# Kernel tuning notes

Measured on AMD Instinct MI355X. Metric: run time of the kernel, lower is better.

Reference implementation:

```python
import jax, jax.numpy as jnp
import numpy as np

B, S, D, H = 2, 2048, 1024, 16
DH = D // H  # head dim = 64


def setup_inputs() -> dict:
    key0 = jax.random.key(0)
    ks = jax.random.split(key0, 12)
    wscale = 0.02
    inp = {
        "query": jax.random.normal(ks[0], (B, S, D), jnp.float32),
        "key": jax.random.normal(ks[1], (B, S, D), jnp.float32),
        "value": jax.random.normal(ks[2], (B, S, D), jnp.float32),
        "mask": jnp.zeros((B, 1, 1, S), jnp.float32),  # 1.0 = masked position
        "Wq": jax.random.normal(ks[3], (D, D), jnp.float32) * wscale,
        "bq": jnp.zeros((D,), jnp.float32),
        "Wk": jax.random.normal(ks[4], (D, D), jnp.float32) * wscale,
        "bk": jnp.zeros((D,), jnp.float32),
        "Wv": jax.random.normal(ks[5], (D, D), jnp.float32) * wscale,
        "bv": jnp.zeros((D,), jnp.float32),
        "Wo": jax.random.normal(ks[6], (D, D), jnp.float32) * wscale,
        "bo": jnp.zeros((D,), jnp.float32),
        "batch_size": B,
    }
    return inp


def _split_heads(x, batch_size):
    # [B, S, D] -> [B, H, S, DH]
    return x.reshape(batch_size, -1, H, DH).transpose(0, 2, 1, 3)


def reference(query, key, value, mask, Wq, bq, Wk, bk, Wv, bv, Wo, bo, batch_size):
    q = _split_heads(query @ Wq + bq, batch_size)  # [B,H,S,DH]
    k = _split_heads(key @ Wk + bk, batch_size)
    v = _split_heads(value @ Wv + bv, batch_size)

    scale = 1.0 / jnp.sqrt(jnp.asarray(DH, q.dtype))
    scores = jnp.einsum("bhqd,bhkd->bhqk", q, k) * scale  # [B,H,S,S]
    scores = scores + mask * jnp.asarray(-1e9, scores.dtype)
    attn = jax.nn.softmax(scores, axis=-1)
    ctx = jnp.einsum("bhqk,bhkd->bhqd", attn, v)  # [B,H,S,DH]

    ctx = ctx.transpose(0, 2, 1, 3).reshape(batch_size, -1, D)  # [B,S,D]
    return ctx @ Wo + bo
```

## Files before the change

kernel.cpp:

```cpp
#include <hip/hip_runtime.h>
#include <hip/hip_bf16.h>

#define BB 2
#define SS 2048
#define DD 1024
#define HH 16
#define DHH 64
#define MM (BB * SS)

typedef unsigned short u16;
using v8s   = __attribute__((ext_vector_type(8))) short;
using f32x4 = __attribute__((ext_vector_type(4))) float;

__device__ __forceinline__ u16 f2bf(float f) {
  unsigned int u = __float_as_uint(f);
  u += 0x7fffu + ((u >> 16) & 1u);
  return (u16)(u >> 16);
}

__device__ __forceinline__ void async_cp16(const u16* g, u16* l) {
  __builtin_amdgcn_global_load_lds(
      (const __attribute__((address_space(1))) unsigned int*)g,
      (__attribute__((address_space(3))) unsigned int*)l, 16, 0, 0);
}

__global__ __launch_bounds__(256) void conv_all(const float* __restrict__ x0,
                                                const float* __restrict__ x1,
                                                const float* __restrict__ x2,
                                                u16* __restrict__ y0,
                                                u16* __restrict__ y1,
                                                u16* __restrict__ y2) {
  const int z = blockIdx.y;
  const float* x = z == 0 ? x0 : (z == 1 ? x1 : x2);
  u16* y = z == 0 ? y0 : (z == 1 ? y1 : y2);
  int i = (blockIdx.x * 256 + threadIdx.x) * 4;
  float4 v = *(const float4*)(x + i);
  ushort4 u;
  u.x = f2bf(v.x); u.y = f2bf(v.y); u.z = f2bf(v.z); u.w = f2bf(v.w);
  *(ushort4*)(y + i) = u;
}

__global__ __launch_bounds__(256) void trans_all(
    const float* __restrict__ W0, const float* __restrict__ W1,
    const float* __restrict__ W2, const float* __restrict__ W3,
    u16* __restrict__ T0, u16* __restrict__ T1,
    u16* __restrict__ T2, u16* __restrict__ T3) {
  const int z = blockIdx.z;
  const float* W = z == 0 ? W0 : (z == 1 ? W1 : (z == 2 ? W2 : W3));
  u16* Wt = z == 0 ? T0 : (z == 1 ? T1 : (z == 2 ? T2 : T3));
  __shared__ u16 T[64][72];
  const int tid = threadIdx.x;
  const int k0 = blockIdx.y * 64, n0 = blockIdx.x * 64;
#pragma unroll
  for (int i = 0; i < 4; i++) {
    int idx = tid + i * 256;
    int r = idx >> 4, c = (idx & 15) * 4;
    float4 x = *(const float4*)(W + (long)(k0 + r) * DD + n0 + c);
    T[c + 0][r] = f2bf(x.x);
    T[c + 1][r] = f2bf(x.y);
    T[c + 2][r] = f2bf(x.z);
    T[c + 3][r] = f2bf(x.w);
  }
  __syncthreads();
#pragma unroll
  for (int i = 0; i < 2; i++) {
    int idx = tid + i * 256;
    int n = idx >> 3, kc = (idx & 7) * 8;
    *(v8s*)(Wt + (long)(n0 + n) * DD + k0 + kc) = *(const v8s*)&T[n][kc];
  }
}

__global__ __launch_bounds__(256, 2) void proj_fused(
    const u16* __restrict__ qb, const u16* __restrict__ kb, const u16* __restrict__ vb,
    const u16* __restrict__ Wqt, const u16* __restrict__ Wkt, const u16* __restrict__ Wvt,
    const float* __restrict__ bq, const float* __restrict__ bk, const float* __restrict__ bv,
    u16* __restrict__ qo, u16* __restrict__ ko, u16* __restrict__ vo) {
  __shared__ u16 As[128 * 32];
  __shared__ u16 Bs[128 * 32];
  const int z = blockIdx.z;
  const u16* A  = z == 0 ? qb : (z == 1 ? kb : vb);
  const u16* Bt = z == 0 ? Wqt : (z == 1 ? Wkt : Wvt);
  const float* bias = z == 0 ? bq : (z == 1 ? bk : bv);
  u16* out = z == 0 ? qo : (z == 1 ? ko : vo);
  const float scale = z == 0 ? 0.125f : 1.0f;

  const int tid = threadIdx.x;
  const int w = tid >> 6, lane = tid & 63;
  const int quad = lane >> 4, lq = lane & 15;
  const int wm = w >> 1, wn = w & 1;
  const int row0 = blockIdx.y * 128, col0 = blockIdx.x * 128;

  f32x4 acc[4][4];
#pragma unroll
  for (int i = 0; i < 4; i++)
#pragma unroll
    for (int j = 0; j < 4; j++)
#pragma unroll
      for (int r = 0; r < 4; r++) acc[i][j][r] = 0.f;

  const int cr = tid >> 2, cc = (tid & 3) * 8;

  for (int k0 = 0; k0 < DD; k0 += 32) {
    __syncthreads();
    async_cp16(A  + (long)(row0 + cr) * DD + k0 + cc,      As + (w * 64) * 8);
    async_cp16(A  + (long)(row0 + 64 + cr) * DD + k0 + cc, As + (256 + w * 64) * 8);
    async_cp16(Bt + (long)(col0 + cr) * DD + k0 + cc,      Bs + (w * 64) * 8);
    async_cp16(Bt + (long)(col0 + 64 + cr) * DD + k0 + cc, Bs + (256 + w * 64) * 8);
    __syncthreads();

    v8s a[4], b[4];
#pragma unroll
    for (int i = 0; i < 4; i++)
      a[i] = *(const v8s*)&As[(wm * 64 + i * 16 + lq) * 32 + quad * 8];
#pragma unroll
    for (int j = 0; j < 4; j++)
      b[j] = *(const v8s*)&Bs[(wn * 64 + j * 16 + lq) * 32 + quad * 8];
#pragma unroll
    for (int i = 0; i < 4; i++)
#pragma unroll
      for (int j = 0; j < 4; j++)
        acc[i][j] = __builtin_amdgcn_mfma_f32_16x16x32_bf16(a[i], b[j], acc[i][j], 0, 0, 0);
  }

#pragma unroll
  for (int i = 0; i < 4; i++)
#pragma unroll
    for (int j = 0; j < 4; j++) {
      int n = col0 + wn * 64 + j * 16 + lq;
      float bi = bias[n];
#pragma unroll
      for (int r = 0; r < 4; r++) {
        int m = row0 + wm * 64 + i * 16 + quad * 4 + r;
        float val = (acc[i][j][r] + bi) * scale;
        int bb = m >> 11, s = m & (SS - 1);
        int hh = n >> 6, d = n & (DHH - 1);
        long off = (z != 2) ? ((long)(bb * HH + hh) * SS + s) * DHH + d
                            : ((long)(bb * HH + hh) * DHH + d) * SS + s;
        out[off] = f2bf(val);
      }
    }
}

__global__ __launch_bounds__(256, 2) void out_gemm(const u16* __restrict__ A,
                                                   const u16* __restrict__ Bt,
                                                   const float* __restrict__ bias,
                                                   float* __restrict__ outp) {
  __shared__ u16 As[64 * 32];
  __shared__ u16 Bs[128 * 32];
  const int tid = threadIdx.x;
  const int w = tid >> 6, lane = tid & 63;
  const int quad = lane >> 4, lq = lane & 15;
  const int wm = w >> 1, wn = w & 1;
  const int row0 = blockIdx.y * 64, col0 = blockIdx.x * 128;

  f32x4 acc[2][4];
#pragma unroll
  for (int i = 0; i < 2; i++)
#pragma unroll
    for (int j = 0; j < 4; j++)
#pragma unroll
      for (int r = 0; r < 4; r++) acc[i][j][r] = 0.f;

  const int cr = tid >> 2, cc = (tid & 3) * 8;

  for (int k0 = 0; k0 < DD; k0 += 32) {
    __syncthreads();
    async_cp16(A  + (long)(row0 + cr) * DD + k0 + cc,      As + (w * 64) * 8);
    async_cp16(Bt + (long)(col0 + cr) * DD + k0 + cc,      Bs + (w * 64) * 8);
    async_cp16(Bt + (long)(col0 + 64 + cr) * DD + k0 + cc, Bs + (256 + w * 64) * 8);
    __syncthreads();

    v8s a[2], b[4];
#pragma unroll
    for (int i = 0; i < 2; i++)
      a[i] = *(const v8s*)&As[(wm * 32 + i * 16 + lq) * 32 + quad * 8];
#pragma unroll
    for (int j = 0; j < 4; j++)
      b[j] = *(const v8s*)&Bs[(wn * 64 + j * 16 + lq) * 32 + quad * 8];
#pragma unroll
    for (int i = 0; i < 2; i++)
#pragma unroll
      for (int j = 0; j < 4; j++)
        acc[i][j] = __builtin_amdgcn_mfma_f32_16x16x32_bf16(a[i], b[j], acc[i][j], 0, 0, 0);
  }

#pragma unroll
  for (int i = 0; i < 2; i++)
#pragma unroll
    for (int j = 0; j < 4; j++) {
      int n = col0 + wn * 64 + j * 16 + lq;
      float bi = bias[n];
#pragma unroll
      for (int r = 0; r < 4; r++) {
        int m = row0 + wm * 32 + i * 16 + quad * 4 + r;
        outp[(long)m * DD + n] = acc[i][j][r] + bi;
      }
    }
}

__global__ __launch_bounds__(256, 2) void attn_flash(
    const u16* __restrict__ qg, const u16* __restrict__ kg,
    const u16* __restrict__ vg, const float* __restrict__ mask,
    u16* __restrict__ ctx) {
  __shared__ u16 Ks[128 * 72];
  __shared__ u16 Vs[64 * 136];
  __shared__ u16 Pts[128 * 136];
  __shared__ float mneg[128];

  const int tid = threadIdx.x;
  const int w = tid >> 6, lane = tid & 63;
  const int quad = lane >> 4, lq = lane & 15;
  const int q0 = blockIdx.x * 128;
  const int h = blockIdx.y, b = blockIdx.z;
  const long hoff = (long)(b * HH + h) * SS * DHH;

  v8s aq[2][2];
#pragma unroll
  for (int qs_ = 0; qs_ < 2; qs_++)
#pragma unroll
    for (int ks_ = 0; ks_ < 2; ks_++)
      aq[qs_][ks_] = *(const v8s*)(qg + hoff +
          (long)(q0 + w * 32 + qs_ * 16 + lq) * DHH + ks_ * 32 + quad * 8);

  f32x4 o[2][4];
  float l_i[2] = {0.f, 0.f};
#pragma unroll
  for (int a = 0; a < 2; a++)
#pragma unroll
    for (int n_ = 0; n_ < 4; n_++)
#pragma unroll
      for (int r = 0; r < 4; r++) o[a][n_][r] = 0.f;

  for (int kv0 = 0; kv0 < SS; kv0 += 128) {
    __syncthreads();
#pragma unroll
    for (int t = 0; t < 4; t++) {
      int c = tid + t * 256;
      *(v8s*)&Ks[(c >> 3) * 72 + (c & 7) * 8] =
          *(const v8s*)(kg + hoff + (long)(kv0 + (c >> 3)) * DHH + (c & 7) * 8);
      *(v8s*)&Vs[(c >> 4) * 136 + (c & 15) * 8] =
          *(const v8s*)(vg + hoff + (long)(c >> 4) * SS + kv0 + (c & 15) * 8);
    }
    if (tid < 32) {
      float4 mm = *(const float4*)(mask + (long)b * SS + kv0 + tid * 4);
      mneg[tid * 4 + 0] = mm.x * -1e9f - 4.0f;
      mneg[tid * 4 + 1] = mm.y * -1e9f - 4.0f;
      mneg[tid * 4 + 2] = mm.z * -1e9f - 4.0f;
      mneg[tid * 4 + 3] = mm.w * -1e9f - 4.0f;
    }
    __syncthreads();

    f32x4 sc[2][8];
#pragma unroll
    for (int qs_ = 0; qs_ < 2; qs_++)
#pragma unroll
      for (int kv_ = 0; kv_ < 8; kv_++)
#pragma unroll
        for (int r = 0; r < 4; r++) sc[qs_][kv_][r] = 0.f;
#pragma unroll
    for (int ks_ = 0; ks_ < 2; ks_++)
#pragma unroll
      for (int kv_ = 0; kv_ < 8; kv_++) {
        v8s ak = *(const v8s*)&Ks[(kv_ * 16 + lq) * 72 + ks_ * 32 + quad * 8];
        sc[0][kv_] = __builtin_amdgcn_mfma_f32_16x16x32_bf16(ak, aq[0][ks_], sc[0][kv_], 0, 0, 0);
        sc[1][kv_] = __builtin_amdgcn_mfma_f32_16x16x32_bf16(ak, aq[1][ks_], sc[1][kv_], 0, 0, 0);
      }

#pragma unroll
    for (int qs_ = 0; qs_ < 2; qs_++) {
      float lsum = 0.f;
      const int prow = (w * 32 + qs_ * 16 + lq) * 136;
#pragma unroll
      for (int kv_ = 0; kv_ < 8; kv_++) {
        f32x4 mv = *(const f32x4*)&mneg[kv_ * 16 + quad * 4];
        float p0 = __expf(sc[qs_][kv_][0] + mv[0]);
        float p1 = __expf(sc[qs_][kv_][1] + mv[1]);
        float p2 = __expf(sc[qs_][kv_][2] + mv[2]);
        float p3 = __expf(sc[qs_][kv_][3] + mv[3]);
        lsum += (p0 + p1) + (p2 + p3);
        ushort4 pk;
        pk.x = f2bf(p0); pk.y = f2bf(p1); pk.z = f2bf(p2); pk.w = f2bf(p3);
        *(ushort4*)&Pts[prow + kv_ * 16 + quad * 4] = pk;
      }
      l_i[qs_] += lsum;
    }

#pragma unroll
    for (int ks2 = 0; ks2 < 4; ks2++) {
      v8s bv[4];
#pragma unroll
      for (int n_ = 0; n_ < 4; n_++)
        bv[n_] = *(const v8s*)&Vs[(n_ * 16 + lq) * 136 + ks2 * 32 + quad * 8];
#pragma unroll
      for (int qs_ = 0; qs_ < 2; qs_++) {
        v8s ap = *(const v8s*)&Pts[(w * 32 + qs_ * 16 + lq) * 136 + ks2 * 32 + quad * 8];
#pragma unroll
        for (int n_ = 0; n_ < 4; n_++)
          o[qs_][n_] = __builtin_amdgcn_mfma_f32_16x16x32_bf16(ap, bv[n_], o[qs_][n_], 0, 0, 0);
      }
    }
  }

#pragma unroll
  for (int qs_ = 0; qs_ < 2; qs_++) {
    float l = l_i[qs_];
    l += __shfl_xor(l, 16);
    l += __shfl_xor(l, 32);
    float inv = 1.0f / l;
    float ir[4];
    ir[0] = __shfl(inv, quad * 4 + 0);
    ir[1] = __shfl(inv, quad * 4 + 1);
    ir[2] = __shfl(inv, quad * 4 + 2);
    ir[3] = __shfl(inv, quad * 4 + 3);
#pragma unroll
    for (int r = 0; r < 4; r++) {
      int s = q0 + w * 32 + qs_ * 16 + quad * 4 + r;
      long base = (long)(b * SS + s) * DD + h * DHH;
#pragma unroll
      for (int n_ = 0; n_ < 4; n_++)
        ctx[base + n_ * 16 + lq] = f2bf(o[qs_][n_][r] * ir[r]);
    }
  }
}

extern "C" void kernel_launch(void* const* d_in, const int* in_sizes, int n_in,
                              void* d_out, int out_size, void* d_ws, size_t ws_size,
                              hipStream_t stream) {
  const float* query = (const float*)d_in[0];
  const float* key   = (const float*)d_in[1];
  const float* value = (const float*)d_in[2];
  const float* mask  = (const float*)d_in[3];
  const float* Wq = (const float*)d_in[4];
  const float* bq = (const float*)d_in[5];
  const float* Wk = (const float*)d_in[6];
  const float* bk = (const float*)d_in[7];
  const float* Wv = (const float*)d_in[8];
  const float* bv = (const float*)d_in[9];
  const float* Wo = (const float*)d_in[10];
  const float* bo = (const float*)d_in[11];

  u16* ws = (u16*)d_ws;
  const long A4 = (long)MM * DD;
  const long W1 = (long)DD * DD;
  u16* qb  = ws;
  u16* kb  = ws + A4;
  u16* vb  = ws + 2 * A4;
  u16* Wqt = ws + 3 * A4;
  u16* Wkt = Wqt + W1;
  u16* Wvt = Wkt + W1;
  u16* Wot = Wvt + W1;
  u16* q_ws   = ws + 3 * A4 + 4 * W1;
  u16* k_ws   = q_ws + A4;
  u16* v_ws   = k_ws + A4;
  u16* ctx_ws = v_ws + A4;

  conv_all<<<dim3(A4 / 1024, 3), 256, 0, stream>>>(query, key, value, qb, kb, vb);
  trans_all<<<dim3(16, 16, 4), 256, 0, stream>>>(Wq, Wk, Wv, Wo, Wqt, Wkt, Wvt, Wot);

  proj_fused<<<dim3(DD / 128, MM / 128, 3), 256, 0, stream>>>(
      qb, kb, vb, Wqt, Wkt, Wvt, bq, bk, bv, q_ws, k_ws, v_ws);

  attn_flash<<<dim3(SS / 128, HH, BB), 256, 0, stream>>>(q_ws, k_ws, v_ws, mask, ctx_ws);

  out_gemm<<<dim3(DD / 128, MM / 64), 256, 0, stream>>>(ctx_ws, Wot, bo, (float*)d_out);
}
```

Measured before the change: 248.7 us.

## Stage projection epilogue through LDS for coalesced stores; use exp2 and packed bf16

The QKV projection epilogue now writes results into a shared-memory tile (aliased with the GEMM staging buffers through a union) and then issues 16-byte coalesced stores in the head-split layout. The V output is written transposed through the tile, which replaces the scattered 2-byte global writes. The attention softmax folds log2(e) into the Q scale and the mask offset so it can use exp2f, and bf16 conversions use the packed hardware conversion intrinsic. The larger shared buffer may reduce occupancy, and the packed conversion's rounding may differ slightly from the manual round-to-nearest-even.

After: 251.8 us. Within noise of the previous version (+1.3%).

```diff
diff --git a/kernel.cpp b/kernel.cpp
--- a/kernel.cpp
+++ b/kernel.cpp
@@ -12,10 +12,17 @@
 using v8s   = __attribute__((ext_vector_type(8))) short;
 using f32x4 = __attribute__((ext_vector_type(4))) float;
 
+#define LOG2E 1.44269504088896340736f
+
 __device__ __forceinline__ u16 f2bf(float f) {
   unsigned int u = __float_as_uint(f);
   u += 0x7fffu + ((u >> 16) & 1u);
   return (u16)(u >> 16);
+}
+
+__device__ __forceinline__ unsigned int pk2(float a, float b) {
+  __hip_bfloat162 h = __float22bfloat162_rn(float2{a, b});
+  return *(unsigned int*)&h;
 }
 
 __device__ __forceinline__ void async_cp16(const u16* g, u16* l) {
@@ -35,9 +42,10 @@
   u16* y = z == 0 ? y0 : (z == 1 ? y1 : y2);
   int i = (blockIdx.x * 256 + threadIdx.x) * 4;
   float4 v = *(const float4*)(x + i);
-  ushort4 u;
-  u.x = f2bf(v.x); u.y = f2bf(v.y); u.z = f2bf(v.z); u.w = f2bf(v.w);
-  *(ushort4*)(y + i) = u;
+  uint2 u;
+  u.x = pk2(v.x, v.y);
+  u.y = pk2(v.z, v.w);
+  *(uint2*)(y + i) = u;
 }
 
 __global__ __launch_bounds__(256) void trans_all(
@@ -75,14 +83,16 @@
     const u16* __restrict__ Wqt, const u16* __restrict__ Wkt, const u16* __restrict__ Wvt,
     const float* __restrict__ bq, const float* __restrict__ bk, const float* __restrict__ bv,
     u16* __restrict__ qo, u16* __restrict__ ko, u16* __restrict__ vo) {
-  __shared__ u16 As[128 * 32];
-  __shared__ u16 Bs[128 * 32];
+  __shared__ union ShU {
+    struct { u16 As[128 * 32]; u16 Bs[128 * 32]; } st;
+    u16 T[128 * 136];
+  } sh;
   const int z = blockIdx.z;
   const u16* A  = z == 0 ? qb : (z == 1 ? kb : vb);
   const u16* Bt = z == 0 ? Wqt : (z == 1 ? Wkt : Wvt);
   const float* bias = z == 0 ? bq : (z == 1 ? bk : bv);
   u16* out = z == 0 ? qo : (z == 1 ? ko : vo);
-  const float scale = z == 0 ? 0.125f : 1.0f;
+  const float scale = z == 0 ? 0.125f * LOG2E : 1.0f;
 
   const int tid = threadIdx.x;
   const int w = tid >> 6, lane = tid & 63;
@@ -102,19 +112,19 @@
 
   for (int k0 = 0; k0 < DD; k0 += 32) {
     __syncthreads();
-    async_cp16(A  + (long)(row0 + cr) * DD + k0 + cc,      As + (w * 64) * 8);
-    async_cp16(A  + (long)(row0 + 64 + cr) * DD + k0 + cc, As + (256 + w * 64) * 8);
-    async_cp16(Bt + (long)(col0 + cr) * DD + k0 + cc,      Bs + (w * 64) * 8);
-    async_cp16(Bt + (long)(col0 + 64 + cr) * DD + k0 + cc, Bs + (256 + w * 64) * 8);
+    async_cp16(A  + (long)(row0 + cr) * DD + k0 + cc,      sh.st.As + (w * 64) * 8);
+    async_cp16(A  + (long)(row0 + 64 + cr) * DD + k0 + cc, sh.st.As + (256 + w * 64) * 8);
+    async_cp16(Bt + (long)(col0 + cr) * DD + k0 + cc,      sh.st.Bs + (w * 64) * 8);
+    async_cp16(Bt + (long)(col0 + 64 + cr) * DD + k0 + cc, sh.st.Bs + (256 + w * 64) * 8);
     __syncthreads();
 
     v8s a[4], b[4];
 #pragma unroll
     for (int i = 0; i < 4; i++)
-      a[i] = *(const v8s*)&As[(wm * 64 + i * 16 + lq) * 32 + quad * 8];
+      a[i] = *(const v8s*)&sh.st.As[(wm * 64 + i * 16 + lq) * 32 + quad * 8];
 #pragma unroll
     for (int j = 0; j < 4; j++)
-      b[j] = *(const v8s*)&Bs[(wn * 64 + j * 16 + lq) * 32 + quad * 8];
+      b[j] = *(const v8s*)&sh.st.Bs[(wn * 64 + j * 16 + lq) * 32 + quad * 8];
 #pragma unroll
     for (int i = 0; i < 4; i++)
 #pragma unroll
@@ -122,23 +132,60 @@
         acc[i][j] = __builtin_amdgcn_mfma_f32_16x16x32_bf16(a[i], b[j], acc[i][j], 0, 0, 0);
   }
 
-#pragma unroll
-  for (int i = 0; i < 4; i++)
+  __syncthreads();
+
+  if (z != 2) {
 #pragma unroll
     for (int j = 0; j < 4; j++) {
-      int n = col0 + wn * 64 + j * 16 + lq;
-      float bi = bias[n];
-#pragma unroll
-      for (int r = 0; r < 4; r++) {
-        int m = row0 + wm * 64 + i * 16 + quad * 4 + r;
-        float val = (acc[i][j][r] + bi) * scale;
-        int bb = m >> 11, s = m & (SS - 1);
-        int hh = n >> 6, d = n & (DHH - 1);
-        long off = (z != 2) ? ((long)(bb * HH + hh) * SS + s) * DHH + d
-                            : ((long)(bb * HH + hh) * DHH + d) * SS + s;
-        out[off] = f2bf(val);
+      int nl = wn * 64 + j * 16 + lq;
+      float bi = bias[col0 + nl];
+#pragma unroll
+      for (int i = 0; i < 4; i++)
+#pragma unroll
+        for (int r = 0; r < 4; r++) {
+          int ml = wm * 64 + i * 16 + quad * 4 + r;
+          sh.T[ml * 136 + nl] = f2bf((acc[i][j][r] + bi) * scale);
+        }
+    }
+    __syncthreads();
+    const int bb = row0 >> 11;
+#pragma unroll
+    for (int t = 0; t < 8; t++) {
+      int c = tid + t * 256;
+      int m = c >> 4, jc = c & 15;
+      int s = (row0 + m) & (SS - 1);
+      int gn = col0 + jc * 8;
+      int hh = gn >> 6, d = gn & (DHH - 1);
+      long off = ((long)(bb * HH + hh) * SS + s) * DHH + d;
+      *(v8s*)(out + off) = *(const v8s*)&sh.T[m * 136 + jc * 8];
+    }
+  } else {
+#pragma unroll
+    for (int j = 0; j < 4; j++) {
+      int nl = wn * 64 + j * 16 + lq;
+      float bi = bias[col0 + nl];
+#pragma unroll
+      for (int i = 0; i < 4; i++) {
+        int ml = wm * 64 + i * 16 + quad * 4;
+        uint2 pk;
+        pk.x = pk2(acc[i][j][0] + bi, acc[i][j][1] + bi);
+        pk.y = pk2(acc[i][j][2] + bi, acc[i][j][3] + bi);
+        *(uint2*)&sh.T[nl * 136 + ml] = pk;
       }
     }
+    __syncthreads();
+    const int bb = row0 >> 11;
+#pragma unroll
+    for (int t = 0; t < 8; t++) {
+      int c = tid + t * 256;
+      int n = c >> 4, jc = c & 15;
+      int gn = col0 + n;
+      int hh = gn >> 6, d = gn & (DHH - 1);
+      int s = (row0 + jc * 8) & (SS - 1);
+      long off = ((long)(bb * HH + hh) * DHH + d) * SS + s;
+      *(v8s*)(out + off) = *(const v8s*)&sh.T[n * 136 + jc * 8];
+    }
+  }
 }
 
 __global__ __launch_bounds__(256, 2) void out_gemm(const u16* __restrict__ A,
@@ -243,10 +290,10 @@
     }
     if (tid < 32) {
       float4 mm = *(const float4*)(mask + (long)b * SS + kv0 + tid * 4);
-      mneg[tid * 4 + 0] = mm.x * -1e9f - 4.0f;
-      mneg[tid * 4 + 1] = mm.y * -1e9f - 4.0f;
-      mneg[tid * 4 + 2] = mm.z * -1e9f - 4.0f;
-      mneg[tid * 4 + 3] = mm.w * -1e9f - 4.0f;
+      mneg[tid * 4 + 0] = (mm.x * -1e9f - 4.0f) * LOG2E;
+      mneg[tid * 4 + 1] = (mm.y * -1e9f - 4.0f) * LOG2E;
+      mneg[tid * 4 + 2] = (mm.z * -1e9f - 4.0f) * LOG2E;
+      mneg[tid * 4 + 3] = (mm.w * -1e9f - 4.0f) * LOG2E;
     }
     __syncthreads();
 
@@ -273,14 +320,15 @@
 #pragma unroll
       for (int kv_ = 0; kv_ < 8; kv_++) {
         f32x4 mv = *(const f32x4*)&mneg[kv_ * 16 + quad * 4];
-        float p0 = __expf(sc[qs_][kv_][0] + mv[0]);
-        float p1 = __expf(sc[qs_][kv_][1] + mv[1]);
-        float p2 = __expf(sc[qs_][kv_][2] + mv[2]);
-        float p3 = __expf(sc[qs_][kv_][3] + mv[3]);
+        float p0 = exp2f(sc[qs_][kv_][0] + mv[0]);
+        float p1 = exp2f(sc[qs_][kv_][1] + mv[1]);
+        float p2 = exp2f(sc[qs_][kv_][2] + mv[2]);
+        float p3 = exp2f(sc[qs_][kv_][3] + mv[3]);
         lsum += (p0 + p1) + (p2 + p3);
-        ushort4 pk;
-        pk.x = f2bf(p0); pk.y = f2bf(p1); pk.z = f2bf(p2); pk.w = f2bf(p3);
-        *(ushort4*)&Pts[prow + kv_ * 16 + quad * 4] = pk;
+        uint2 pk;
+        pk.x = pk2(p0, p1);
+        pk.y = pk2(p2, p3);
+        *(uint2*)&Pts[prow + kv_ * 16 + quad * 4] = pk;
       }
       l_i[qs_] += lsum;
     }
```
